# Kernel tuning notes

Measured on AMD Instinct MI355X. Metric: run time of the kernel, lower is better.

## Reference

```python
import jax, jax.numpy as jnp
import numpy as np

Q_LEN, KV_LEN, N_HEADS, HEAD_DIM = 2048, 4096, 16, 64
NEG_INF = -1e9


def _causal_prefix_mask(q_len, kv_len):
    # query i (global position prefix+i) may attend to keys j <= prefix + i
    prefix = kv_len - q_len
    i = jnp.arange(q_len)[:, None]
    j = jnp.arange(kv_len)[None, :]
    allowed = j <= (prefix + i)
    return jnp.where(allowed, 0.0, NEG_INF).astype(jnp.float32)[None, None]  # [1,1,q,kv]


def setup_inputs() -> dict:
    key = jax.random.key(0)
    kq, kk, kv = jax.random.split(key, 3)
    query = jax.random.normal(kq, (1, N_HEADS, Q_LEN, HEAD_DIM), dtype=jnp.float32)
    k = jax.random.normal(kk, (1, N_HEADS, KV_LEN, HEAD_DIM), dtype=jnp.float32)
    v = jax.random.normal(kv, (1, N_HEADS, KV_LEN, HEAD_DIM), dtype=jnp.float32)
    attn_mask = _causal_prefix_mask(Q_LEN, KV_LEN)
    return {"query": query, "key": k, "value": v, "attn_mask": attn_mask}


def reference(query, key, value, attn_mask):
    # Equivalent math of SlicedFusedSDPA.forward: chunked causal SDPA with
    # online-softmax merge == one full masked softmax attention.
    # scale=None -> 1/sqrt(head_dim); dropout_p=0; is_causal=True encoded in attn_mask.
    scale = 1.0 / np.sqrt(query.shape[-1]).astype(np.float32)
    scores = jnp.einsum('bhqd,bhkd->bhqk', query, key) * scale + attn_mask  # [B,H,Q,KV]
    probs = jax.nn.softmax(scores, axis=-1)
    out = jnp.einsum('bhqk,bhkd->bhqd', probs, value)
    return out.astype(query.dtype)
```

## Files before the change

kernel.cpp:

```cpp
#include <hip/hip_runtime.h>
#include <hip/hip_bf16.h>

#define NH 16
#define QL 2048
#define KVL 4096
#define DH 64
#define PREFIX (KVL - QL)
#define NT 64
#define TUS 8192
#define SCALE 0.18033688011112043f

typedef __attribute__((ext_vector_type(8))) _Float16 f16x8;
typedef __attribute__((ext_vector_type(8))) short short8;
typedef __attribute__((ext_vector_type(4))) float f32x4;
typedef __attribute__((ext_vector_type(16))) float f32x16;
typedef unsigned int u32;

static __device__ __forceinline__ float exp2_fast(float x) {
    float r; asm("v_exp_f32 %0, %1" : "=v"(r) : "v"(x)); return r;
}
static __device__ __forceinline__ u32 pkrtz(float lo, float hi) {
    u32 r; asm("v_cvt_pkrtz_f16_f32 %0, %1, %2" : "=v"(r) : "v"(lo), "v"(hi)); return r;
}
static __device__ __forceinline__ void plswap(u32& x, u32& y) {
    asm("v_permlane32_swap_b32 %0, %1" : "+v"(x), "+v"(y));
}
#define MFMAH(a, b, c) __builtin_amdgcn_mfma_f32_32x32x16_f16(a, b, c, 0, 0, 0)

static __device__ __forceinline__ ushort f2bf(float x) {
    union { float f; u32 u; } v; v.f = x;
    u32 r = v.u + 0x7fffu + ((v.u >> 16) & 1u);
    return (ushort)(r >> 16);
}
static __device__ __forceinline__ float bf2f(ushort h) {
    union { u32 u; float f; } v; v.u = ((u32)h) << 16;
    return v.f;
}

__global__ void convKV(const float* __restrict__ K, const float* __restrict__ V,
                       ushort* __restrict__ ws) {
    const int half = blockIdx.x >> 11;
    const int gid  = (blockIdx.x & 2047) * 256 + threadIdx.x;
    const int lane = gid & 63;
    const int fidx = (gid >> 6) & 7;
    const int tile = (gid >> 9) & 63;
    const int h    = gid >> 15;
    const int lq = lane & 31, hi = lane >> 5;
    f16x8 o;
    if (half == 0) {
        const int t = fidx >> 2, ks = fidx & 3;
        const int kv = tile * 64 + t * 32 + lq;
        const float* src = K + ((size_t)h * KVL + kv) * DH + ks * 16 + hi * 8;
        const float4 a = *(const float4*)src;
        const float4 b = *(const float4*)(src + 4);
        const float v[8] = {a.x, a.y, a.z, a.w, b.x, b.y, b.z, b.w};
        #pragma unroll
        for (int j = 0; j < 8; ++j) o[j] = (_Float16)v[j];
        *(f16x8*)(ws + (size_t)(h * NT + tile) * TUS + fidx * 512 + lane * 8) = o;
    } else {
        const int dt = fidx >> 2, ks = fidx & 3;
        const int d  = dt * 32 + lq;
        const float* src = V + ((size_t)h * KVL + tile * 64 + ks * 16 + hi * 8) * DH + d;
        #pragma unroll
        for (int j = 0; j < 8; ++j) o[j] = (_Float16)src[j * DH];
        *(f16x8*)(ws + (size_t)(h * NT + tile) * TUS + 4096 + fidx * 512 + lane * 8) = o;
    }
}

template<int NSPLIT>
__global__ __launch_bounds__(256, 4)
void sdpa_main(const float* __restrict__ Q, const ushort* __restrict__ ws,
               float* __restrict__ part)
{
    const int tid  = threadIdx.x;
    const int lane = tid & 63;
    const int w    = tid >> 6;
    const int lq   = lane & 31;
    const int hi   = lane >> 5;

    const int bid = blockIdx.x;
    const int xcd = bid & 7;
    const int k   = bid >> 3;
    int h, qwA, sp;
    if constexpr (NSPLIT == 4) {
        const int hsub = k & 1;
        const int kk   = k >> 1;
        h   = xcd * 2 + hsub;
        qwA = kk >> 1;
        sp  = (w >> 1) * 2 + (kk & 1);
    } else {
        h   = xcd * 2 + (k & 1);
        qwA = k >> 1;
        sp  = w >> 1;
    }
    const int qw = (w & 1) ? (63 - qwA) : qwA;
    const int qb = qw * 32;

    const int ntt = (PREFIX + qb + 32) >> 5;
    const int t0  = (ntt * sp) / NSPLIT;
    const int t1  = (ntt * (sp + 1)) / NSPLIT;

    f16x8 qh[4];
    {
        const float* qp = Q + ((size_t)h * QL + qb + lq) * DH + hi * 8;
        #pragma unroll
        for (int ks = 0; ks < 4; ++ks) {
            const float4 a = *(const float4*)(qp + ks * 16);
            const float4 b = *(const float4*)(qp + ks * 16 + 4);
            const float vv[8] = {a.x, a.y, a.z, a.w, b.x, b.y, b.z, b.w};
            #pragma unroll
            for (int jj = 0; jj < 8; ++jj)
                qh[ks][jj] = (_Float16)(vv[jj] * SCALE);
        }
    }

    f32x16 oacc[2];
    #pragma unroll
    for (int dt = 0; dt < 2; ++dt)
        #pragma unroll
        for (int r = 0; r < 16; ++r) oacc[dt][r] = 0.f;
    float m = 0.0f, lsum = 0.f;

    const ushort* hb = ws + (size_t)h * NT * TUS + lane * 8;

    for (int it = t0; it < t1; ++it) {
        const int s = it & 1;
        const ushort* b64 = hb + (size_t)(it >> 1) * TUS;
        const ushort* bK  = b64 + s * 2048;
        const ushort* bV  = b64 + 4096 + s * 1024;

        f16x8 kf[4], vf[4];
        #pragma unroll
        for (int f = 0; f < 4; ++f) kf[f] = *(const f16x8*)(bK + f * 512);
        #pragma unroll
        for (int dt = 0; dt < 2; ++dt)
            #pragma unroll
            for (int kv2 = 0; kv2 < 2; ++kv2)
                vf[dt * 2 + kv2] = *(const f16x8*)(bV + dt * 2048 + kv2 * 512);

        f32x16 sT;
        #pragma unroll
        for (int r = 0; r < 16; ++r) sT[r] = 0.f;
        __builtin_amdgcn_s_setprio(1);
        #pragma unroll
        for (int ks = 0; ks < 4; ++ks) sT = MFMAH(kf[ks], qh[ks], sT);
        __builtin_amdgcn_s_setprio(0);

        const int kv0 = it * 32;
        if (kv0 + 32 > PREFIX + qb) {
            const int kvlim = PREFIX + qb + lq - kv0;
            #pragma unroll
            for (int r = 0; r < 16; ++r) {
                const int c = (r & 3) + 8 * (r >> 2) + 4 * hi;
                if (c > kvlim) sT[r] = -1e30f;
            }
        }

        float tmx[8];
        #pragma unroll
        for (int i = 0; i < 8; ++i) tmx[i] = fmaxf(sT[i], sT[i + 8]);
        #pragma unroll
        for (int ss = 4; ss > 0; ss >>= 1)
            #pragma unroll
            for (int i = 0; i < ss; ++i) tmx[i] = fmaxf(tmx[i], tmx[i + ss]);
        float mx = fmaxf(tmx[0], __shfl_xor(tmx[0], 32));
        if (__any(mx > m + 8.0f)) {
            const float mn  = fmaxf(m, mx);
            const float fsc = exp2_fast(m - mn);
            lsum *= fsc;
            #pragma unroll
            for (int dt = 0; dt < 2; ++dt)
                #pragma unroll
                for (int r = 0; r < 16; ++r) oacc[dt][r] *= fsc;
            m = mn;
        }
        #pragma unroll
        for (int r = 0; r < 16; ++r) sT[r] = exp2_fast(sT[r] - m);
        float ts[8];
        #pragma unroll
        for (int i = 0; i < 8; ++i) ts[i] = sT[i] + sT[i + 8];
        #pragma unroll
        for (int ss = 4; ss > 0; ss >>= 1)
            #pragma unroll
            for (int i = 0; i < ss; ++i) ts[i] += ts[i + ss];
        lsum += ts[0];

        u32 x0 = pkrtz(sT[0],  sT[1]);
        u32 x1 = pkrtz(sT[2],  sT[3]);
        u32 y0 = pkrtz(sT[4],  sT[5]);
        u32 y1 = pkrtz(sT[6],  sT[7]);
        u32 x2 = pkrtz(sT[8],  sT[9]);
        u32 x3 = pkrtz(sT[10], sT[11]);
        u32 y2 = pkrtz(sT[12], sT[13]);
        u32 y3 = pkrtz(sT[14], sT[15]);
        plswap(x0, y0); plswap(x1, y1);
        plswap(x2, y2); plswap(x3, y3);
        union { u32 u[4]; f16x8 v; } p0, p1;
        p0.u[0] = x0; p0.u[1] = x1; p0.u[2] = y0; p0.u[3] = y1;
        p1.u[0] = x2; p1.u[1] = x3; p1.u[2] = y2; p1.u[3] = y3;

        __builtin_amdgcn_s_setprio(1);
        oacc[0] = MFMAH(vf[0], p0.v, oacc[0]);
        oacc[0] = MFMAH(vf[1], p1.v, oacc[0]);
        oacc[1] = MFMAH(vf[2], p0.v, oacc[1]);
        oacc[1] = MFMAH(vf[3], p1.v, oacc[1]);
        __builtin_amdgcn_s_setprio(0);
    }

    const float ltot = lsum + __shfl_xor(lsum, 32);
    float* pr = part + ((size_t)(sp * NH + h) * QL + qb + lq) * 68;
    #pragma unroll
    for (int dt = 0; dt < 2; ++dt)
        #pragma unroll
        for (int a = 0; a < 4; ++a) {
            f32x4 o;
            #pragma unroll
            for (int jj = 0; jj < 4; ++jj) o[jj] = oacc[dt][a * 4 + jj];
            *(f32x4*)(pr + dt * 32 + a * 8 + hi * 4) = o;
        }
    if (hi == 0) { pr[64] = m; pr[65] = ltot; }
}

template<int NSPLIT>
__global__ void combineN(const float* __restrict__ part, float* __restrict__ O) {
    const int row = blockIdx.x * 4 + (threadIdx.x >> 6);
    const int d   = threadIdx.x & 63;
    float mj[NSPLIT], lj[NSPLIT], M = -1e30f;
    #pragma unroll
    for (int j = 0; j < NSPLIT; ++j) {
        const float* p = part + ((size_t)j * NH * QL + row) * 68;
        mj[j] = p[64]; lj[j] = p[65];
        M = fmaxf(M, mj[j]);
    }
    float num = 0.f, den = 0.f;
    #pragma unroll
    for (int j = 0; j < NSPLIT; ++j) {
        const float* p = part + ((size_t)j * NH * QL + row) * 68;
        const float wj = exp2f(mj[j] - M);
        num += wj * p[d];
        den += wj * lj[j];
    }
    O[(size_t)row * DH + d] = num / den;
}

#define QT 64
#define KBf 32
#define KSTR 72
#define VSTR 40
#define PSTR 40
#define SCALE_E 0.125f

__global__ __launch_bounds__(256, 2)
void sdpa_fallback(const float* __restrict__ Q, const float* __restrict__ K,
                   const float* __restrict__ V, float* __restrict__ O)
{
    __shared__ ushort sKh[KBf][KSTR];
    __shared__ ushort sKl[KBf][KSTR];
    __shared__ ushort sVt[DH][VSTR];
    __shared__ ushort sPf[4][16][PSTR];

    const int tid  = threadIdx.x;
    const int lane = tid & 63;
    const int w    = tid >> 6;
    const int h    = blockIdx.y;
    const int q0   = blockIdx.x * QT;
    const int qb   = q0 + w * 16;
    const int lrow = lane & 15;
    const int lgrp = lane >> 4;

    short8 qh[2], ql[2];
    {
        const float* qp = Q + ((size_t)h * QL + (qb + lrow)) * DH;
        #pragma unroll
        for (int dh = 0; dh < 2; ++dh) {
            const int d0 = dh * 32 + lgrp * 8;
            #pragma unroll
            for (int jj = 0; jj < 8; ++jj) {
                float x = qp[d0 + jj] * SCALE_E;
                ushort hb = f2bf(x);
                qh[dh][jj] = (short)hb;
                ql[dh][jj] = (short)f2bf(x - bf2f(hb));
            }
        }
    }

    f32x4 oacc[4];
    float m_r[4], l_r[4];
    #pragma unroll
    for (int n = 0; n < 4; ++n) { oacc[n][0]=0.f; oacc[n][1]=0.f; oacc[n][2]=0.f; oacc[n][3]=0.f; }
    #pragma unroll
    for (int r = 0; r < 4; ++r) { m_r[r] = -1e30f; l_r[r] = 0.f; }

    const int nkv = min(KVL, PREFIX + q0 + QT);

    for (int kv0 = 0; kv0 < nkv; kv0 += KBf) {
        __syncthreads();
        {
            const int r  = tid >> 3;
            const int d0 = (tid & 7) * 8;
            const float* kp = K + ((size_t)h * KVL + (kv0 + r)) * DH + d0;
            const float* vp = V + ((size_t)h * KVL + (kv0 + r)) * DH + d0;
            short8 vh, vl;
            #pragma unroll
            for (int jj = 0; jj < 8; ++jj) {
                float x = kp[jj];
                ushort hb = f2bf(x);
                vh[jj] = (short)hb;
                vl[jj] = (short)f2bf(x - bf2f(hb));
            }
            *(short8*)&sKh[r][d0] = vh;
            *(short8*)&sKl[r][d0] = vl;
            #pragma unroll
            for (int jj = 0; jj < 8; ++jj)
                sVt[d0 + jj][r] = f2bf(vp[jj]);
        }
        __syncthreads();

        f32x4 s[2];
        #pragma unroll
        for (int t = 0; t < 2; ++t) { s[t][0]=0.f; s[t][1]=0.f; s[t][2]=0.f; s[t][3]=0.f; }
        #pragma unroll
        for (int t = 0; t < 2; ++t) {
            #pragma unroll
            for (int dh = 0; dh < 2; ++dh) {
                const short8 kh = *(const short8*)&sKh[t*16 + lrow][dh*32 + lgrp*8];
                const short8 kl = *(const short8*)&sKl[t*16 + lrow][dh*32 + lgrp*8];
                s[t] = __builtin_amdgcn_mfma_f32_16x16x32_bf16(qh[dh], kh, s[t], 0, 0, 0);
                s[t] = __builtin_amdgcn_mfma_f32_16x16x32_bf16(qh[dh], kl, s[t], 0, 0, 0);
                s[t] = __builtin_amdgcn_mfma_f32_16x16x32_bf16(ql[dh], kh, s[t], 0, 0, 0);
            }
        }

        if (kv0 + KBf > PREFIX + qb) {
            #pragma unroll
            for (int t = 0; t < 2; ++t)
                #pragma unroll
                for (int r = 0; r < 4; ++r) {
                    const int kv = kv0 + t*16 + lrow;
                    const int q  = qb + lgrp*4 + r;
                    if (kv > PREFIX + q) s[t][r] = -1e30f;
                }
        }

        float tmax[4];
        #pragma unroll
        for (int r = 0; r < 4; ++r) tmax[r] = fmaxf(s[0][r], s[1][r]);
        #pragma unroll
        for (int off = 1; off <= 8; off <<= 1)
            #pragma unroll
            for (int r = 0; r < 4; ++r) tmax[r] = fmaxf(tmax[r], __shfl_xor(tmax[r], off, 64));

        float f[4];
        #pragma unroll
        for (int r = 0; r < 4; ++r) {
            const float mn = fmaxf(m_r[r], tmax[r]);
            f[r] = __expf(m_r[r] - mn);
            m_r[r] = mn;
        }
        #pragma unroll
        for (int t = 0; t < 2; ++t)
            #pragma unroll
            for (int r = 0; r < 4; ++r) s[t][r] = __expf(s[t][r] - m_r[r]);

        float rs[4];
        #pragma unroll
        for (int r = 0; r < 4; ++r) rs[r] = s[0][r] + s[1][r];
        #pragma unroll
        for (int off = 1; off <= 8; off <<= 1)
            #pragma unroll
            for (int r = 0; r < 4; ++r) rs[r] += __shfl_xor(rs[r], off, 64);
        #pragma unroll
        for (int r = 0; r < 4; ++r) l_r[r] = l_r[r] * f[r] + rs[r];
        #pragma unroll
        for (int n = 0; n < 4; ++n)
            #pragma unroll
            for (int r = 0; r < 4; ++r) oacc[n][r] *= f[r];

        #pragma unroll
        for (int t = 0; t < 2; ++t)
            #pragma unroll
            for (int r = 0; r < 4; ++r)
                sPf[w][lgrp*4 + r][t*16 + lrow] = f2bf(s[t][r]);
        asm volatile("s_waitcnt lgkmcnt(0)" ::: "memory");
        __builtin_amdgcn_sched_barrier(0);

        const short8 pa = *(const short8*)&sPf[w][lrow][lgrp*8];
        #pragma unroll
        for (int n = 0; n < 4; ++n) {
            const short8 vb = *(const short8*)&sVt[n*16 + lrow][lgrp*8];
            oacc[n] = __builtin_amdgcn_mfma_f32_16x16x32_bf16(pa, vb, oacc[n], 0, 0, 0);
        }
    }

    float inv[4];
    #pragma unroll
    for (int r = 0; r < 4; ++r) inv[r] = 1.0f / l_r[r];
    float* op = O + ((size_t)h * QL + qb) * DH;
    #pragma unroll
    for (int n = 0; n < 4; ++n)
        #pragma unroll
        for (int r = 0; r < 4; ++r)
            op[(lgrp*4 + r) * DH + n*16 + lrow] = oacc[n][r] * inv[r];
}

extern "C" void kernel_launch(void* const* d_in, const int* in_sizes, int n_in,
                              void* d_out, int out_size, void* d_ws, size_t ws_size,
                              hipStream_t stream) {
    const float* Q = (const float*)d_in[0];
    const float* K = (const float*)d_in[1];
    const float* V = (const float*)d_in[2];
    float* O = (float*)d_out;
    const size_t KVWS = (size_t)NH * NT * TUS * 2;
    const size_t PART = (size_t)NH * QL * 68 * 4;
    ushort* wsKV = (ushort*)d_ws;
    float*  part = (float*)((char*)d_ws + KVWS);

    if (ws_size >= KVWS + 4 * PART) {
        hipLaunchKernelGGL(convKV, dim3(4096), dim3(256), 0, stream, K, V, wsKV);
        hipLaunchKernelGGL(sdpa_main<4>, dim3(1024), dim3(256), 0, stream, Q, wsKV, part);
        hipLaunchKernelGGL(combineN<4>, dim3(8192), dim3(256), 0, stream, part, O);
    } else if (ws_size >= KVWS + 2 * PART) {
        hipLaunchKernelGGL(convKV, dim3(4096), dim3(256), 0, stream, K, V, wsKV);
        hipLaunchKernelGGL(sdpa_main<2>, dim3(512), dim3(256), 0, stream, Q, wsKV, part);
        hipLaunchKernelGGL(combineN<2>, dim3(8192), dim3(256), 0, stream, part, O);
    } else {
        hipLaunchKernelGGL(sdpa_fallback, dim3(32, 16), dim3(256), 0, stream, Q, K, V, O);
    }
}
```

Before: 68.17 us.

## Prefetch K tiles into LDS asynchronously and store fp16 normalized partials

K tiles are now staged two iterations ahead into per-wave LDS double buffers using global_load_lds, with an explicit vmcnt wait, so K load latency overlaps with compute. V is still read directly from global memory. Partial outputs are normalized per split and written as packed fp16 along with a single log-sum-exp value, which roughly halves partial traffic and simplifies the combine kernel. The cost is lower precision in the partials and the fragility of a hand-counted vmcnt wait, since V loads are issued between the stages.

After: 68.13 us. About the same (-0.1%).

```diff
diff --git a/kernel.cpp b/kernel.cpp
--- a/kernel.cpp
+++ b/kernel.cpp
@@ -8,9 +8,11 @@
 #define PREFIX (KVL - QL)
 #define NT 64
 #define TUS 8192
+#define PSTR32 34
 #define SCALE 0.18033688011112043f
 
 typedef __attribute__((ext_vector_type(8))) _Float16 f16x8;
+typedef __attribute__((ext_vector_type(2))) _Float16 f16x2;
 typedef __attribute__((ext_vector_type(8))) short short8;
 typedef __attribute__((ext_vector_type(4))) float f32x4;
 typedef __attribute__((ext_vector_type(16))) float f32x16;
@@ -26,6 +28,12 @@
     asm("v_permlane32_swap_b32 %0, %1" : "+v"(x), "+v"(y));
 }
 #define MFMAH(a, b, c) __builtin_amdgcn_mfma_f32_32x32x16_f16(a, b, c, 0, 0, 0)
+
+static __device__ __forceinline__ void gload_lds16(const ushort* g, ushort* l) {
+    __builtin_amdgcn_global_load_lds(
+        (const __attribute__((address_space(1))) u32*)g,
+        (__attribute__((address_space(3))) u32*)l, 16, 0, 0);
+}
 
 static __device__ __forceinline__ ushort f2bf(float x) {
     union { float f; u32 u; } v; v.f = x;
@@ -72,6 +80,8 @@
 void sdpa_main(const float* __restrict__ Q, const ushort* __restrict__ ws,
                float* __restrict__ part)
 {
+    __shared__ ushort lds[4][2][2048];
+
     const int tid  = threadIdx.x;
     const int lane = tid & 63;
     const int w    = tid >> 6;
@@ -123,28 +133,47 @@
 
     const ushort* hb = ws + (size_t)h * NT * TUS + lane * 8;
 
+    #define KSRC(IT) (hb + (size_t)((IT) >> 1) * TUS + ((IT) & 1) * 2048)
+    #define KSTAGE(IT, B) do {                                             \
+        const ushort* _s = KSRC(IT);                                       \
+        ushort* _d = &lds[w][(B)][0];                                      \
+        gload_lds16(_s,        _d);                                        \
+        gload_lds16(_s + 512,  _d + 512);                                  \
+        gload_lds16(_s + 1024, _d + 1024);                                 \
+        gload_lds16(_s + 1536, _d + 1536);                                 \
+    } while (0)
+
+    KSTAGE(t0, t0 & 1);
+    if (t0 + 1 < t1) KSTAGE(t0 + 1, (t0 + 1) & 1);
+
     for (int it = t0; it < t1; ++it) {
-        const int s = it & 1;
-        const ushort* b64 = hb + (size_t)(it >> 1) * TUS;
-        const ushort* bK  = b64 + s * 2048;
-        const ushort* bV  = b64 + 4096 + s * 1024;
-
-        f16x8 kf[4], vf[4];
-        #pragma unroll
-        for (int f = 0; f < 4; ++f) kf[f] = *(const f16x8*)(bK + f * 512);
-        #pragma unroll
-        for (int dt = 0; dt < 2; ++dt)
-            #pragma unroll
-            for (int kv2 = 0; kv2 < 2; ++kv2)
-                vf[dt * 2 + kv2] = *(const f16x8*)(bV + dt * 2048 + kv2 * 512);
+        asm volatile("s_waitcnt vmcnt(4)" ::: "memory");
+        __builtin_amdgcn_sched_barrier(0);
+
+        const ushort* bV = hb + (size_t)(it >> 1) * TUS + 4096 + (it & 1) * 1024;
+        f16x8 vf[4];
+        vf[0] = *(const f16x8*)(bV);
+        vf[1] = *(const f16x8*)(bV + 512);
+        vf[2] = *(const f16x8*)(bV + 2048);
+        vf[3] = *(const f16x8*)(bV + 2560);
+
+        const ushort* kb = &lds[w][it & 1][lane * 8];
+        f16x8 kf0 = *(const f16x8*)(kb);
+        f16x8 kf1 = *(const f16x8*)(kb + 512);
+        f16x8 kf2 = *(const f16x8*)(kb + 1024);
+        f16x8 kf3 = *(const f16x8*)(kb + 1536);
 
         f32x16 sT;
         #pragma unroll
         for (int r = 0; r < 16; ++r) sT[r] = 0.f;
         __builtin_amdgcn_s_setprio(1);
-        #pragma unroll
-        for (int ks = 0; ks < 4; ++ks) sT = MFMAH(kf[ks], qh[ks], sT);
+        sT = MFMAH(kf0, qh[0], sT);
+        sT = MFMAH(kf1, qh[1], sT);
+        sT = MFMAH(kf2, qh[2], sT);
+        sT = MFMAH(kf3, qh[3], sT);
         __builtin_amdgcn_s_setprio(0);
+
+        if (it + 2 < t1) KSTAGE(it + 2, it & 1);
 
         const int kv0 = it * 32;
         if (kv0 + 32 > PREFIX + qb) {
@@ -206,41 +235,48 @@
         oacc[1] = MFMAH(vf[3], p1.v, oacc[1]);
         __builtin_amdgcn_s_setprio(0);
     }
+    #undef KSTAGE
+    #undef KSRC
 
     const float ltot = lsum + __shfl_xor(lsum, 32);
-    float* pr = part + ((size_t)(sp * NH + h) * QL + qb + lq) * 68;
+    const float linv = 1.0f / ltot;
+    u32* pr = (u32*)part + ((size_t)(sp * NH + h) * QL + qb + lq) * PSTR32;
     #pragma unroll
     for (int dt = 0; dt < 2; ++dt)
         #pragma unroll
         for (int a = 0; a < 4; ++a) {
-            f32x4 o;
-            #pragma unroll
-            for (int jj = 0; jj < 4; ++jj) o[jj] = oacc[dt][a * 4 + jj];
-            *(f32x4*)(pr + dt * 32 + a * 8 + hi * 4) = o;
-        }
-    if (hi == 0) { pr[64] = m; pr[65] = ltot; }
-}
-
-template<int NSPLIT>
-__global__ void combineN(const float* __restrict__ part, float* __restrict__ O) {
-    const int row = blockIdx.x * 4 + (threadIdx.x >> 6);
-    const int d   = threadIdx.x & 63;
-    float mj[NSPLIT], lj[NSPLIT], M = -1e30f;
-    #pragma unroll
-    for (int j = 0; j < NSPLIT; ++j) {
-        const float* p = part + ((size_t)j * NH * QL + row) * 68;
-        mj[j] = p[64]; lj[j] = p[65];
-        M = fmaxf(M, mj[j]);
-    }
-    float num = 0.f, den = 0.f;
-    #pragma unroll
-    for (int j = 0; j < NSPLIT; ++j) {
-        const float* p = part + ((size_t)j * NH * QL + row) * 68;
-        const float wj = exp2f(mj[j] - M);
-        num += wj * p[d];
-        den += wj * lj[j];
-    }
-    O[(size_t)row * DH + d] = num / den;
+            const u32 w0 = pkrtz(oacc[dt][a * 4 + 0] * linv, oacc[dt][a * 4 + 1] * linv);
+            const u32 w1 = pkrtz(oacc[dt][a * 4 + 2] * linv, oacc[dt][a * 4 + 3] * linv);
+            pr[dt * 16 + a * 4 + hi * 2 + 0] = w0;
+            pr[dt * 16 + a * 4 + hi * 2 + 1] = w1;
+        }
+    if (hi == 0) pr[32] = __float_as_uint(m + log2f(ltot));
+}
+
+template<int N>
+__global__ void combineH(const u32* __restrict__ part, float* __restrict__ O) {
+    const int r = blockIdx.x * 8 + (threadIdx.x >> 5);
+    const int p = threadIdx.x & 31;
+    float g[N], M = -1e30f;
+    #pragma unroll
+    for (int j = 0; j < N; ++j) {
+        g[j] = __uint_as_float(part[((size_t)j * NH * QL + r) * PSTR32 + 32]);
+        M = fmaxf(M, g[j]);
+    }
+    float a0 = 0.f, a1 = 0.f, wsum = 0.f;
+    #pragma unroll
+    for (int j = 0; j < N; ++j) {
+        const float wj = exp2f(g[j] - M);
+        union { u32 u; f16x2 h; } v;
+        v.u = part[((size_t)j * NH * QL + r) * PSTR32 + p];
+        a0 += wj * (float)v.h[0];
+        a1 += wj * (float)v.h[1];
+        wsum += wj;
+    }
+    const float inv = 1.0f / wsum;
+    float* op = O + (size_t)r * DH + p * 2;
+    op[0] = a0 * inv;
+    op[1] = a1 * inv;
 }
 
 #define QT 64
@@ -410,19 +446,19 @@
     const float* K = (const float*)d_in[1];
     const float* V = (const float*)d_in[2];
     float* O = (float*)d_out;
-    const size_t KVWS = (size_t)NH * NT * TUS * 2;
-    const size_t PART = (size_t)NH * QL * 68 * 4;
+    const size_t KVWS  = (size_t)NH * NT * TUS * 2;
+    const size_t PARTH = (size_t)NH * QL * PSTR32 * 4;
     ushort* wsKV = (ushort*)d_ws;
     float*  part = (float*)((char*)d_ws + KVWS);
 
-    if (ws_size >= KVWS + 4 * PART) {
+    if (ws_size >= KVWS + 4 * PARTH) {
         hipLaunchKernelGGL(convKV, dim3(4096), dim3(256), 0, stream, K, V, wsKV);
         hipLaunchKernelGGL(sdpa_main<4>, dim3(1024), dim3(256), 0, stream, Q, wsKV, part);
-        hipLaunchKernelGGL(combineN<4>, dim3(8192), dim3(256), 0, stream, part, O);
-    } else if (ws_size >= KVWS + 2 * PART) {
+        hipLaunchKernelGGL(combineH<4>, dim3(4096), dim3(256), 0, stream, (const u32*)part, O);
+    } else if (ws_size >= KVWS + 2 * PARTH) {
         hipLaunchKernelGGL(convKV, dim3(4096), dim3(256), 0, stream, K, V, wsKV);
         hipLaunchKernelGGL(sdpa_main<2>, dim3(512), dim3(256), 0, stream, Q, wsKV, part);
-        hipLaunchKernelGGL(combineN<2>, dim3(8192), dim3(256), 0, stream, part, O);
+        hipLaunchKernelGGL(combineH<2>, dim3(4096), dim3(256), 0, stream, (const u32*)part, O);
     } else {
         hipLaunchKernelGGL(sdpa_fallback, dim3(32, 16), dim3(256), 0, stream, Q, K, V, O);
     }
```
